# Kernel tuning notes

Hardware: AMD Instinct MI355X
Metric: run time of the kernel (lower is better)

Reference implementation:

```python
import jax, jax.numpy as jnp
import numpy as np

LRELU_SLOPE = 0.2
ACT_GAIN = np.float32(np.sqrt(2.0))  # bias_act lrelu gain in StyleGAN2


def _per_sample_conv3x3(x, w):
    """Grouped-conv-as-batch trick: per-sample 3x3 conv.
    x: [B, C, H, W], w: [B, O, C, 3, 3] -> [B, O, H, W] (padding=1)."""
    def one(xi, wi):
        return jax.lax.conv_general_dilated(
            xi[None], wi, window_strides=(1, 1), padding=[(1, 1), (1, 1)],
            dimension_numbers=('NCHW', 'OIHW', 'NCHW'))[0]
    return jax.vmap(one)(x, w)


def setup_inputs() -> dict:
    key = jax.random.key(0)
    ks = jax.random.split(key, 10)
    B, C, R, W_DIM, IMG_C = 16, 512, 64, 512, 3
    inv_sqrt_c = np.float32(1.0 / np.sqrt(W_DIM))
    return {
        'ws': jax.random.normal(ks[0], (B, 2, W_DIM), jnp.float32),
        'const': jax.random.normal(ks[1], (C, R, R), jnp.float32),
        'conv_w': jax.random.normal(ks[2], (C, C, 3, 3), jnp.float32),
        'conv_b': jnp.zeros((C,), jnp.float32),
        'conv_aff_w': jax.random.normal(ks[3], (C, W_DIM), jnp.float32) * inv_sqrt_c,
        'conv_aff_b': jnp.ones((C,), jnp.float32),
        'noise_const': jax.random.normal(ks[4], (R, R), jnp.float32),
        'noise_strength': jnp.full((1,), 0.1, jnp.float32),
        'rgb_w': jax.random.normal(ks[5], (IMG_C, C, 1, 1), jnp.float32),
        'rgb_b': jnp.zeros((IMG_C,), jnp.float32),
        'rgb_aff_w': jax.random.normal(ks[6], (C, W_DIM), jnp.float32) * inv_sqrt_c,
        'rgb_aff_b': jnp.ones((C,), jnp.float32),
    }


def reference(ws, const, conv_w, conv_b, conv_aff_w, conv_aff_b,
              noise_const, noise_strength, rgb_w, rgb_b, rgb_aff_w, rgb_aff_b):
    B = ws.shape[0]
    # const input broadcast to batch (in_channels == 0 block)
    x = jnp.broadcast_to(const[None], (B,) + const.shape)

    # --- SynthesisLayer: modulated_conv2d (demodulate=True, fused_modconv=True) ---
    s = ws[:, 0] @ conv_aff_w.T + conv_aff_b                    # [B, C] styles
    w = conv_w[None] * s[:, None, :, None, None]                # [B, O, C, 3, 3] modulate
    dcoefs = jax.lax.rsqrt(jnp.sum(jnp.square(w), axis=(2, 3, 4)) + 1e-8)  # [B, O]
    w = w * dcoefs[:, :, None, None, None]                      # demodulate
    x = _per_sample_conv3x3(x, w)                               # grouped conv trick
    x = x + noise_const[None, None] * noise_strength            # fused noise add
    x = jax.nn.leaky_relu(x + conv_b[None, :, None, None], LRELU_SLOPE) * ACT_GAIN

    # --- ToRGBLayer: modulated 1x1 conv, demodulate=False ---
    weight_gain = np.float32(1.0 / np.sqrt(conv_w.shape[1]))    # 1/sqrt(in_ch*kh*kw)
    s2 = (ws[:, 1] @ rgb_aff_w.T + rgb_aff_b) * weight_gain     # [B, C]
    img = jnp.einsum('bchw,oc,bc->bohw', x, rgb_w[:, :, 0, 0], s2)
    img = img + rgb_b[None, :, None, None]
    return x, img
```

## Files before the change

kernel.cpp:

```cpp
#include <hip/hip_runtime.h>
#include <hip/hip_bf16.h>

typedef __attribute__((ext_vector_type(8))) short short8;
typedef __attribute__((ext_vector_type(4))) float f32x4;

#define LRELU_SLOPE 0.2f
#define ACT_GAIN 1.41421356237309515f
#define WG_RGB 0.04419417382415922f

__device__ __forceinline__ void glds16(const short* g, short* l) {
    __builtin_amdgcn_global_load_lds(
        (const __attribute__((address_space(1))) unsigned int*)g,
        (__attribute__((address_space(3))) unsigned int*)l, 16, 0, 0);
}

__global__ void k_init(__hip_bfloat16* __restrict__ Ypad,
                       const float* __restrict__ rgb_b, float* __restrict__ img) {
    int blk = blockIdx.x, tid = threadIdx.x;
    if (blk < 1040) {
        int gslot = blk*4 + (tid >> 6);
        int b = gslot / 260;
        int cell = gslot - b*260;
        int h, w;
        if (cell < 66)       { h = 0;          w = cell; }
        else if (cell < 132) { h = 65;         w = cell - 66; }
        else if (cell < 196) { h = cell - 131; w = 0; }
        else                 { h = cell - 195; w = 65; }
        short8 z = {};
        *(short8*)((short*)Ypad + (((b*66 + h)*66) + w)*512 + (tid & 63)*8) = z;
    } else {
        int blk2 = blk - 1040;
        #pragma unroll
        for (int j = 0; j < 4; ++j) {
            int f4 = blk2*1024 + j*256 + tid;
            int b3 = f4 >> 10;
            int o3 = b3 % 3;
            float v = rgb_b[o3];
            f32x4 vv = {v, v, v, v};
            *(f32x4*)(img + f4*4) = vv;
        }
    }
}

__global__ void k_styles(const float* __restrict__ wsin,
                         const float* __restrict__ caw, const float* __restrict__ cab,
                         const float* __restrict__ raw_, const float* __restrict__ rab,
                         float* __restrict__ sbuf, float* __restrict__ s2buf) {
    int b = blockIdx.x, which = blockIdx.y;
    int tid = threadIdx.x, lane = tid & 63, wv = tid >> 6;
    const float* aw = which ? raw_ : caw;
    const float* ab = which ? rab : cab;
    float scale = which ? WG_RGB : 1.0f;
    float* op = which ? s2buf : sbuf;
    __shared__ float wsv[512];
    wsv[tid]       = wsin[(b*2 + which)*512 + tid];
    wsv[tid + 256] = wsin[(b*2 + which)*512 + tid + 256];
    __syncthreads();
    for (int c = wv; c < 512; c += 4) {
        float p = 0.f;
        #pragma unroll
        for (int kk = 0; kk < 8; ++kk)
            p += aw[c*512 + kk*64 + lane] * wsv[kk*64 + lane];
        #pragma unroll
        for (int off = 32; off; off >>= 1) p += __shfl_down(p, off, 64);
        if (lane == 0) op[b*512 + c] = (p + ab[c]) * scale;
    }
}

__global__ __launch_bounds__(256) void k_prepw(const float* __restrict__ conv_w,
                        float* __restrict__ w2sum, __hip_bfloat16* __restrict__ Abf) {
    int o = blockIdx.x, tid = threadIdx.x;
    __shared__ float wrow[4608];
    const f32x4* src = (const f32x4*)(conv_w + o*4608);
    #pragma unroll
    for (int r = 0; r < 5; ++r) {
        int idx = tid + (r << 8);
        if (idx < 1152) *(f32x4*)&wrow[idx*4] = src[idx];
    }
    __syncthreads();
    #pragma unroll
    for (int j = 0; j < 2; ++j) {
        int c = tid + (j << 8);
        float sum = 0.f;
        #pragma unroll
        for (int t = 0; t < 9; ++t) {
            float v = wrow[c*9 + t];
            sum += v*v;
            Abf[(t*512 + o)*512 + c] = __float2bfloat16(v);
        }
        w2sum[o*512 + c] = sum;
    }
}

__global__ __launch_bounds__(256) void k_dcoef(const float* __restrict__ sbuf,
                                               const float* __restrict__ w2sum,
                                               const float* __restrict__ s2buf,
                                               const float* __restrict__ rgb_w,
                                               float* __restrict__ dcoef,
                                               float* __restrict__ rgbc) {
    int gw = blockIdx.x*4 + (threadIdx.x >> 6);
    int lane = threadIdx.x & 63;
    int b = gw >> 9, o = gw & 511;
    float acc = 0.f;
    #pragma unroll
    for (int i = 0; i < 8; ++i) {
        int c = (i << 6) + lane;
        float sv = sbuf[(b << 9) + c];
        acc += sv*sv*w2sum[(o << 9) + c];
    }
    #pragma unroll
    for (int off = 32; off; off >>= 1) acc += __shfl_down(acc, off, 64);
    if (lane == 0) dcoef[(b << 9) + o] = rsqrtf(acc + 1e-8f);
    if (blockIdx.x < 96) {
        int flat = blockIdx.x*256 + threadIdx.x;
        int bb = flat / 1536;
        int r  = flat - bb*1536;
        int c  = r & 511;
        rgbc[flat] = rgb_w[r] * s2buf[bb*512 + c];
    }
}

__global__ void k_ypad(const float* __restrict__ cst, const float* __restrict__ sbuf,
                       __hip_bfloat16* __restrict__ Ypad) {
    int b = blockIdx.x >> 6, h = blockIdx.x & 63, tid = threadIdx.x;
    __shared__ float tile[64][65];
    for (int cc = 0; cc < 8; ++cc) {
        int c0 = cc << 6;
        #pragma unroll
        for (int it = 0; it < 16; ++it) {
            int cl = (it << 2) + (tid >> 6);
            int w = tid & 63;
            tile[cl][w] = cst[(c0 + cl)*4096 + (h << 6) + w];
        }
        __syncthreads();
        #pragma unroll
        for (int it = 0; it < 16; ++it) {
            int flat = (it << 8) + tid;
            int w = flat >> 6, cl = flat & 63;
            float v = sbuf[(b << 9) + c0 + cl] * tile[cl][w];
            Ypad[(((b*66 + h + 1)*66) + (w + 1))*512 + c0 + cl] = __float2bfloat16(v);
        }
        __syncthreads();
    }
}

__global__ __launch_bounds__(256, 2) void conv_gemm(
    const short* __restrict__ Abf,
    const short* __restrict__ Ypad,
    const float* __restrict__ dcoef,
    const float* __restrict__ noise,
    const float* __restrict__ nstr,
    const float* __restrict__ bias,
    const float* __restrict__ rgbc,
    float* __restrict__ xout,
    float* __restrict__ img)
{
    __shared__ short Aring[16384];
    __shared__ short Bh2[16896];
    __shared__ float red[128][3][2];
    int tid = threadIdx.x, lane = tid & 63, wv = tid >> 6;

    int blk = blockIdx.x;
    int xcd = blk & 7, idx = blk >> 3;
    int mblk = xcd & 3;
    int nblk = idx | ((xcd >> 2) << 8);
    int b  = nblk >> 5;
    int n0 = (nblk & 31) << 7;
    int o0 = mblk << 7;
    int h0 = n0 >> 6;

    int bgofs[4];
    #pragma unroll
    for (int r = 0; r < 4; ++r) {
        int i = tid + (r << 8);
        int p = i >> 2;
        int hl = p / 66;
        int w  = p - hl*66;
        int q  = (i & 3) ^ ((p >> 1) & 3);
        bgofs[r] = (((b*66 + h0 + hl)*66) + w)*512 + q*8;
    }
    int i4 = 1024 + (lane & 31);
    int p4 = i4 >> 2;
    int hl4 = p4 / 66;
    int w4 = p4 - hl4*66;
    int q4 = (i4 & 3) ^ ((p4 >> 1) & 3);
    int bgofs4 = (((b*66 + h0 + hl4)*66) + w4)*512 + q4*8;

    int aofs[2];
    #pragma unroll
    for (int r = 0; r < 2; ++r) {
        int s = tid + (r << 8);
        int row = s >> 2;
        int q = (s & 3) ^ ((row >> 1) & 3);
        aofs[r] = ((o0 + row) << 9) + q*8;
    }

    int quad = lane >> 4, ml = lane & 15;
    int sa = (quad ^ ((ml >> 1) & 3)) << 3;
    int mw = (wv & 1) << 6, nw = (wv >> 1) << 6;
    int nh = nw >> 6;
    short* BW0 = Bh2 + ((tid & ~63) << 3);
    short* AW0 = Aring + (wv << 9);

    f32x4 acc[4][4] = {};

    #pragma unroll
    for (int r = 0; r < 4; ++r) glds16(Ypad + bgofs[r], BW0 + (r << 11));
    if (lane < 32) glds16(Ypad + bgofs4, Bh2 + 8192);
    #pragma unroll
    for (int t = 0; t < 3; ++t) {
        glds16(Abf + (t << 18) + aofs[0], AW0 + t*4096);
        glds16(Abf + (t << 18) + aofs[1], AW0 + t*4096 + 2048);
    }
    asm volatile("s_waitcnt vmcnt(4)" ::: "memory");
    __builtin_amdgcn_s_barrier();

    for (int ch = 0; ch < 16; ++ch) {
        int c0 = ch << 5;
        int half = ch & 1;
        const short* Bbase = Bh2 + (half ? 8448 : 0);
        short* BWn  = Bh2 + (half ? 0 : 8448) + ((tid & ~63) << 3);
        short* Brem = Bh2 + (half ? 0 : 8448) + 8192;
        int c0n = (c0 + 32) & 511;
        int rb = ch & 3;
        #pragma unroll
        for (int tap = 0; tap < 9; ++tap) {
            int rr = (rb + tap) & 3;
            int rw = (rb + tap + 3) & 3;
            int tapP = (tap < 6) ? tap + 3 : tap - 6;
            int c0P  = (tap < 6) ? c0 : c0n;
            const short* asrc = Abf + (tapP << 18) + c0P;
            glds16(asrc + aofs[0], AW0 + rw*4096);
            glds16(asrc + aofs[1], AW0 + rw*4096 + 2048);
            if (tap < 4)
                glds16(Ypad + bgofs[tap] + c0n, BWn + (tap << 11));
            if (tap == 4) {
                if (lane < 32) glds16(Ypad + bgofs4 + c0n, Brem);
            }
            int dh = tap / 3, tl = tap % 3;
            const short* Ar = Aring + rr*4096;
            int pb = (nh + dh)*66 + ml + tl;
            int swz = (quad ^ ((pb >> 1) & 3)) << 3;
            short8 af[4], bf[4];
            #pragma unroll
            for (int i = 0; i < 4; ++i) {
                af[i] = *(const short8*)(Ar + (mw + ml + i*16)*32 + sa);
                bf[i] = *(const short8*)(Bbase + (pb + i*16)*32 + swz);
            }
            __builtin_amdgcn_s_setprio(1);
            #pragma unroll
            for (int mi = 0; mi < 4; ++mi)
                #pragma unroll
                for (int ni = 0; ni < 4; ++ni)
                    acc[mi][ni] = __builtin_amdgcn_mfma_f32_16x16x32_bf16(af[mi], bf[ni], acc[mi][ni], 0, 0, 0);
            __builtin_amdgcn_s_setprio(0);
            {
                constexpr int VM[9] = {5, 6, 7, 7, 7, 6, 5, 4, 4};
                asm volatile("s_waitcnt vmcnt(%0)" :: "i"(VM[tap]) : "memory");
            }
            __builtin_amdgcn_s_barrier();
        }
    }

    float ns = nstr[0];
    float pr[4][3] = {};
    #pragma unroll
    for (int mi = 0; mi < 4; ++mi) {
        int ob = o0 + mw + mi*16 + (quad << 2);
        f32x4 dc  = *(const f32x4*)(dcoef + (b << 9) + ob);
        f32x4 bs4 = *(const f32x4*)(bias + ob);
        f32x4 rc0 = *(const f32x4*)(rgbc + b*1536 + ob);
        f32x4 rc1 = *(const f32x4*)(rgbc + b*1536 + 512 + ob);
        f32x4 rc2 = *(const f32x4*)(rgbc + b*1536 + 1024 + ob);
        #pragma unroll
        for (int ni = 0; ni < 4; ++ni) {
            int hw = n0 + nw + ni*16 + ml;
            float nz = noise[hw] * ns;
            #pragma unroll
            for (int r = 0; r < 4; ++r) {
                float v = acc[mi][ni][r] * dc[r] + nz + bs4[r];
                v = (v < 0.0f ? LRELU_SLOPE * v : v) * ACT_GAIN;
                xout[(((b << 9) + ob + r) << 12) + hw] = v;
                pr[ni][0] += v * rc0[r];
                pr[ni][1] += v * rc1[r];
                pr[ni][2] += v * rc2[r];
            }
        }
    }
    #pragma unroll
    for (int ni = 0; ni < 4; ++ni)
        #pragma unroll
        for (int o3 = 0; o3 < 3; ++o3) {
            float v = pr[ni][o3];
            v += __shfl_down(v, 16, 64);
            v += __shfl_down(v, 32, 64);
            pr[ni][o3] = v;
        }
    if (lane < 16) {
        #pragma unroll
        for (int ni = 0; ni < 4; ++ni)
            #pragma unroll
            for (int o3 = 0; o3 < 3; ++o3)
                red[nw + ni*16 + ml][o3][wv & 1] = pr[ni][o3];
    }
    __syncthreads();
    for (int p = tid; p < 384; p += 256) {
        int o3 = p >> 7, hwl = p & 127;
        float v = red[hwl][o3][0] + red[hwl][o3][1];
        atomicAdd(img + ((b*3 + o3) << 12) + n0 + hwl, v);
    }
}

extern "C" void kernel_launch(void* const* d_in, const int* in_sizes, int n_in,
                              void* d_out, int out_size, void* d_ws, size_t ws_size,
                              hipStream_t stream) {
    (void)in_sizes; (void)n_in; (void)out_size; (void)ws_size;
    const float* wsin   = (const float*)d_in[0];
    const float* cst    = (const float*)d_in[1];
    const float* conv_w = (const float*)d_in[2];
    const float* conv_b = (const float*)d_in[3];
    const float* caw    = (const float*)d_in[4];
    const float* cab    = (const float*)d_in[5];
    const float* noise  = (const float*)d_in[6];
    const float* nstr   = (const float*)d_in[7];
    const float* rgb_w  = (const float*)d_in[8];
    const float* rgb_b  = (const float*)d_in[9];
    const float* raw_   = (const float*)d_in[10];
    const float* rab    = (const float*)d_in[11];

    char* wsb = (char*)d_ws;
    float* sbuf   = (float*)(wsb + 0);
    float* s2buf  = (float*)(wsb + 32768);
    float* dcoef  = (float*)(wsb + 65536);
    float* rgbc   = (float*)(wsb + 98304);
    float* w2sum  = (float*)(wsb + 196608);
    __hip_bfloat16* Abf  = (__hip_bfloat16*)(wsb + 1245184);
    __hip_bfloat16* Ypad = (__hip_bfloat16*)(wsb + 5963776);

    float* xout = (float*)d_out;
    float* img  = xout + 33554432;

    k_init<<<1088, 256, 0, stream>>>(Ypad, rgb_b, img);
    k_styles<<<dim3(16, 2), 256, 0, stream>>>(wsin, caw, cab, raw_, rab, sbuf, s2buf);
    k_prepw<<<512, 256, 0, stream>>>(conv_w, w2sum, Abf);
    k_dcoef<<<2048, 256, 0, stream>>>(sbuf, w2sum, s2buf, rgb_w, dcoef, rgbc);
    k_ypad<<<1024, 256, 0, stream>>>(cst, sbuf, Ypad);
    conv_gemm<<<2048, 256, 0, stream>>>((const short*)Abf, (const short*)Ypad,
                                        dcoef, noise, nstr, conv_b, rgbc, xout, img);
}
```

Before: 648.1 us.

## Double-buffer MFMA register fragments to overlap LDS reads with matrix math

Restructures the main conv GEMM loop so the LDS-to-register fragment loads for the next tap are issued before the MFMAs of the current tap, using two register fragment buffers. The channel loop is unrolled by two so buffer half pointers become compile-time constants, and a sched_barrier pins the ordering. The vmcnt wait thresholds are adjusted to match the new issue order. This targets LDS read latency that was exposed before each tap's MFMAs, at the cost of extra VGPRs and larger code.

Result: faster. 593.2 us (-8.5%).

```diff
diff --git a/kernel.cpp b/kernel.cpp
--- a/kernel.cpp
+++ b/kernel.cpp
@@ -186,81 +186,111 @@
     int q4 = (i4 & 3) ^ ((p4 >> 1) & 3);
     int bgofs4 = (((b*66 + h0 + hl4)*66) + w4)*512 + q4*8;
 
-    int aofs[2];
-    #pragma unroll
-    for (int r = 0; r < 2; ++r) {
-        int s = tid + (r << 8);
-        int row = s >> 2;
-        int q = (s & 3) ^ ((row >> 1) & 3);
-        aofs[r] = ((o0 + row) << 9) + q*8;
+    int aofs0, aofs1;
+    {
+        int s0 = tid,       r0 = s0 >> 2, q0 = (s0 & 3) ^ ((r0 >> 1) & 3);
+        int s1 = tid + 256, r1 = s1 >> 2, q1 = (s1 & 3) ^ ((r1 >> 1) & 3);
+        aofs0 = ((o0 + r0) << 9) + q0*8;
+        aofs1 = ((o0 + r1) << 9) + q1*8;
     }
 
     int quad = lane >> 4, ml = lane & 15;
     int sa = (quad ^ ((ml >> 1) & 3)) << 3;
     int mw = (wv & 1) << 6, nw = (wv >> 1) << 6;
     int nh = nw >> 6;
-    short* BW0 = Bh2 + ((tid & ~63) << 3);
+    const short* H0 = Bh2;
+    const short* H1 = Bh2 + 8448;
+    short* BW0h = Bh2 + ((tid & ~63) << 3);
+    short* BW1h = BW0h + 8448;
+    short* Brem0 = Bh2 + 8192;
+    short* Brem1 = Bh2 + 8448 + 8192;
     short* AW0 = Aring + (wv << 9);
 
     f32x4 acc[4][4] = {};
-
-    #pragma unroll
-    for (int r = 0; r < 4; ++r) glds16(Ypad + bgofs[r], BW0 + (r << 11));
-    if (lane < 32) glds16(Ypad + bgofs4, Bh2 + 8192);
+    short8 fa[2][4], fb[2][4];
+
+    #pragma unroll
+    for (int r = 0; r < 4; ++r) glds16(Ypad + bgofs[r], BW0h + (r << 11));
+    if (lane < 32) glds16(Ypad + bgofs4, Brem0);
     #pragma unroll
     for (int t = 0; t < 3; ++t) {
-        glds16(Abf + (t << 18) + aofs[0], AW0 + t*4096);
-        glds16(Abf + (t << 18) + aofs[1], AW0 + t*4096 + 2048);
-    }
-    asm volatile("s_waitcnt vmcnt(4)" ::: "memory");
+        glds16(Abf + (t << 18) + aofs0, AW0 + t*4096);
+        glds16(Abf + (t << 18) + aofs1, AW0 + t*4096 + 2048);
+    }
+    asm volatile("s_waitcnt vmcnt(2)" ::: "memory");
     __builtin_amdgcn_s_barrier();
-
-    for (int ch = 0; ch < 16; ++ch) {
-        int c0 = ch << 5;
-        int half = ch & 1;
-        const short* Bbase = Bh2 + (half ? 8448 : 0);
-        short* BWn  = Bh2 + (half ? 0 : 8448) + ((tid & ~63) << 3);
-        short* Brem = Bh2 + (half ? 0 : 8448) + 8192;
-        int c0n = (c0 + 32) & 511;
-        int rb = ch & 3;
-        #pragma unroll
-        for (int tap = 0; tap < 9; ++tap) {
-            int rr = (rb + tap) & 3;
-            int rw = (rb + tap + 3) & 3;
-            int tapP = (tap < 6) ? tap + 3 : tap - 6;
-            int c0P  = (tap < 6) ? c0 : c0n;
-            const short* asrc = Abf + (tapP << 18) + c0P;
-            glds16(asrc + aofs[0], AW0 + rw*4096);
-            glds16(asrc + aofs[1], AW0 + rw*4096 + 2048);
-            if (tap < 4)
-                glds16(Ypad + bgofs[tap] + c0n, BWn + (tap << 11));
-            if (tap == 4) {
-                if (lane < 32) glds16(Ypad + bgofs4 + c0n, Brem);
-            }
-            int dh = tap / 3, tl = tap % 3;
-            const short* Ar = Aring + rr*4096;
-            int pb = (nh + dh)*66 + ml + tl;
-            int swz = (quad ^ ((pb >> 1) & 3)) << 3;
-            short8 af[4], bf[4];
-            #pragma unroll
-            for (int i = 0; i < 4; ++i) {
-                af[i] = *(const short8*)(Ar + (mw + ml + i*16)*32 + sa);
-                bf[i] = *(const short8*)(Bbase + (pb + i*16)*32 + swz);
-            }
-            __builtin_amdgcn_s_setprio(1);
-            #pragma unroll
-            for (int mi = 0; mi < 4; ++mi)
-                #pragma unroll
-                for (int ni = 0; ni < 4; ++ni)
-                    acc[mi][ni] = __builtin_amdgcn_mfma_f32_16x16x32_bf16(af[mi], bf[ni], acc[mi][ni], 0, 0, 0);
-            __builtin_amdgcn_s_setprio(0);
-            {
-                constexpr int VM[9] = {5, 6, 7, 7, 7, 6, 5, 4, 4};
-                asm volatile("s_waitcnt vmcnt(%0)" :: "i"(VM[tap]) : "memory");
-            }
-            __builtin_amdgcn_s_barrier();
-        }
-    }
+    {
+        int pb0 = nh*66 + ml;
+        int swz0 = (quad ^ ((pb0 >> 1) & 3)) << 3;
+        #pragma unroll
+        for (int i = 0; i < 4; ++i) {
+            fa[0][i] = *(const short8*)(Aring + (mw + ml + i*16)*32 + sa);
+            fb[0][i] = *(const short8*)(H0 + (pb0 + i*16)*32 + swz0);
+        }
+    }
+
+    constexpr int VMP[9] = {3, 4, 4, 4, 4, 3, 2, 2, 2};
+
+#define PHASE(TAP, CUR, C0, C0N, RB, BC, BN, BWN, BRM)                          \
+    {                                                                           \
+        constexpr int TAPN = ((TAP) + 1) % 9;                                   \
+        constexpr int NXT = (CUR) ^ 1;                                          \
+                                           \
+        int rrN = ((RB) + (TAP) + 1) & 3;                                       \
+        const short* ArN = Aring + rrN*4096;                                    \
+        const short* BbN = ((TAP) == 8) ? (BN) : (BC);                          \
+        int pbN = (nh + TAPN/3)*66 + ml + TAPN%3;                               \
+        int swzN = (quad ^ ((pbN >> 1) & 3)) << 3;                              \
+        _Pragma("unroll")                                                       \
+        for (int i = 0; i < 4; ++i) {                                           \
+            fa[NXT][i] = *(const short8*)(ArN + (mw + ml + i*16)*32 + sa);      \
+            fb[NXT][i] = *(const short8*)(BbN + (pbN + i*16)*32 + swzN);        \
+        }                                                                       \
+                \
+        {                                                                       \
+            constexpr int TAPP = ((TAP) < 6) ? (TAP) + 3 : (TAP) - 6;           \
+            const short* asrc = Abf + (TAPP << 18) + (((TAP) < 6) ? (C0) : (C0N)); \
+            int rw = ((RB) + (TAP) + 3) & 3;                                    \
+            glds16(asrc + aofs0, AW0 + rw*4096);                                \
+            glds16(asrc + aofs1, AW0 + rw*4096 + 2048);                         \
+        }                                                                       \
+        if ((TAP) < 4) glds16(Ypad + bgofs[(TAP)] + (C0N), (BWN) + ((TAP) << 11)); \
+        if ((TAP) == 4) { if (lane < 32) glds16(Ypad + bgofs4 + (C0N), (BRM)); } \
+        __builtin_amdgcn_sched_barrier(0);                                      \
+        __builtin_amdgcn_s_setprio(1);                                          \
+        _Pragma("unroll")                                                       \
+        for (int mi = 0; mi < 4; ++mi)                                          \
+            _Pragma("unroll")                                                   \
+            for (int ni = 0; ni < 4; ++ni)                                      \
+                acc[mi][ni] = __builtin_amdgcn_mfma_f32_16x16x32_bf16(          \
+                    fa[(CUR)][mi], fb[(CUR)][ni], acc[mi][ni], 0, 0, 0);        \
+        __builtin_amdgcn_s_setprio(0);                                          \
+        asm volatile("s_waitcnt vmcnt(%0)" :: "i"(VMP[(TAP)]) : "memory");      \
+        __builtin_amdgcn_s_barrier();                                           \
+    }
+
+#define CHUNK9(PAR, C0, C0N, RB, BC, BN, BWN, BRM)                              \
+    PHASE(0, ((0 + (PAR)) & 1), C0, C0N, RB, BC, BN, BWN, BRM)                  \
+    PHASE(1, ((1 + (PAR)) & 1), C0, C0N, RB, BC, BN, BWN, BRM)                  \
+    PHASE(2, ((2 + (PAR)) & 1), C0, C0N, RB, BC, BN, BWN, BRM)                  \
+    PHASE(3, ((3 + (PAR)) & 1), C0, C0N, RB, BC, BN, BWN, BRM)                  \
+    PHASE(4, ((4 + (PAR)) & 1), C0, C0N, RB, BC, BN, BWN, BRM)                  \
+    PHASE(5, ((5 + (PAR)) & 1), C0, C0N, RB, BC, BN, BWN, BRM)                  \
+    PHASE(6, ((6 + (PAR)) & 1), C0, C0N, RB, BC, BN, BWN, BRM)                  \
+    PHASE(7, ((7 + (PAR)) & 1), C0, C0N, RB, BC, BN, BWN, BRM)                  \
+    PHASE(8, ((8 + (PAR)) & 1), C0, C0N, RB, BC, BN, BWN, BRM)
+
+    for (int cc = 0; cc < 8; ++cc) {
+        int c0e = cc << 6;
+        int rbe = (cc << 1) & 3;
+        CHUNK9(0, c0e, c0e + 32, rbe, H0, H1, BW1h, Brem1)
+        int c0o = c0e + 32;
+        int c0no = (c0e + 64) & 511;
+        int rbo = (rbe + 1) & 3;
+        CHUNK9(1, c0o, c0no, rbo, H1, H0, BW0h, Brem0)
+    }
+#undef PHASE
+#undef CHUNK9
 
     float ns = nstr[0];
     float pr[4][3] = {};
```

## Enlarge conv GEMM tiles to 256x256 with 32x32 MFMA and fragment double-buffering

Applied to the files above, without the earlier changes.

Restructures the implicit-GEMM conv kernel from 128x128 tiles with 4 waves to 256x256 tiles with 8 waves (512 threads, 512 blocks). It switches from 16x16x32 to 32x32x16 bf16 MFMA and splits each tap into two K-halves whose LDS fragment loads are double-buffered against the MFMAs. The goal is higher arithmetic intensity per LDS and global byte and better latency hiding. In exchange it needs much more LDS and register pressure (acc now 128 floats per lane), and the grid has fewer blocks per CU.

Result: faster. 574.3 us (-11.4%).

```diff
diff --git a/kernel.cpp b/kernel.cpp
--- a/kernel.cpp
+++ b/kernel.cpp
@@ -3,6 +3,7 @@
 
 typedef __attribute__((ext_vector_type(8))) short short8;
 typedef __attribute__((ext_vector_type(4))) float f32x4;
+typedef __attribute__((ext_vector_type(16))) float f32x16;
 
 #define LRELU_SLOPE 0.2f
 #define ACT_GAIN 1.41421356237309515f
@@ -144,7 +145,7 @@
     }
 }
 
-__global__ __launch_bounds__(256, 2) void conv_gemm(
+__global__ __launch_bounds__(512, 2) void conv_gemm(
     const short* __restrict__ Abf,
     const short* __restrict__ Ypad,
     const float* __restrict__ dcoef,
@@ -155,159 +156,216 @@
     float* __restrict__ xout,
     float* __restrict__ img)
 {
-    __shared__ short Aring[16384];
-    __shared__ short Bh2[16896];
-    __shared__ float red[128][3][2];
+    __shared__ short Aring[32768];
+    __shared__ short Bh2[25344];
+    __shared__ float red[256][3][2];
+
     int tid = threadIdx.x, lane = tid & 63, wv = tid >> 6;
+    int wr = wv >> 2, wc = wv & 3;
+    int ml32 = lane & 31, hi = lane >> 5;
 
     int blk = blockIdx.x;
     int xcd = blk & 7, idx = blk >> 3;
-    int mblk = xcd & 3;
-    int nblk = idx | ((xcd >> 2) << 8);
-    int b  = nblk >> 5;
-    int n0 = (nblk & 31) << 7;
-    int o0 = mblk << 7;
-    int h0 = n0 >> 6;
-
-    int bgofs[4];
-    #pragma unroll
-    for (int r = 0; r < 4; ++r) {
-        int i = tid + (r << 8);
-        int p = i >> 2;
-        int hl = p / 66;
-        int w  = p - hl*66;
-        int q  = (i & 3) ^ ((p >> 1) & 3);
-        bgofs[r] = (((b*66 + h0 + hl)*66) + w)*512 + q*8;
-    }
-    int i4 = 1024 + (lane & 31);
-    int p4 = i4 >> 2;
-    int hl4 = p4 / 66;
-    int w4 = p4 - hl4*66;
-    int q4 = (i4 & 3) ^ ((p4 >> 1) & 3);
-    int bgofs4 = (((b*66 + h0 + hl4)*66) + w4)*512 + q4*8;
-
-    int aofs[2];
+    int v = xcd * 64 + idx;
+    int mblk = v & 1, nblk = v >> 1;
+    int b = nblk >> 4;
+    int hw0 = (nblk & 15) << 8;
+    int h0 = hw0 >> 6;
+    int o0 = mblk << 8;
+
+    int bgofs[3];
+    #pragma unroll
+    for (int r = 0; r < 3; ++r) {
+        int i = tid + (r << 9);
+        int pos = i >> 2;
+        int hl = pos / 66;
+        int ww = pos - hl*66;
+        int q  = (i & 3) ^ ((pos >> 1) & 3);
+        bgofs[r] = (((b*66 + h0 + hl)*66) + ww)*512 + q*8;
+    }
+    int pos4 = 384 + (lane >> 2);
+    int q4 = (lane & 3) ^ ((pos4 >> 1) & 3);
+    int bg4 = ((b*66 + h0 + 5)*66 + (pos4 - 330))*512 + q4*8;
+
+    int agofs[2];
     #pragma unroll
     for (int r = 0; r < 2; ++r) {
-        int s = tid + (r << 8);
+        int s = tid + (r << 9);
         int row = s >> 2;
         int q = (s & 3) ^ ((row >> 1) & 3);
-        aofs[r] = ((o0 + row) << 9) + q*8;
-    }
-
-    int quad = lane >> 4, ml = lane & 15;
-    int sa = (quad ^ ((ml >> 1) & 3)) << 3;
-    int mw = (wv & 1) << 6, nw = (wv >> 1) << 6;
-    int nh = nw >> 6;
-    short* BW0 = Bh2 + ((tid & ~63) << 3);
-    short* AW0 = Aring + (wv << 9);
-
-    f32x4 acc[4][4] = {};
-
-    #pragma unroll
-    for (int r = 0; r < 4; ++r) glds16(Ypad + bgofs[r], BW0 + (r << 11));
-    if (lane < 32) glds16(Ypad + bgofs4, Bh2 + 8192);
+        agofs[r] = ((o0 + row) << 9) + q*8;
+    }
+
+    int aro[4], arx[4];
+    #pragma unroll
+    for (int mi = 0; mi < 4; ++mi) {
+        int row = wr*128 + mi*32 + ml32;
+        aro[mi] = row*32;
+        arx[mi] = (row >> 1) & 3;
+    }
+    int pb0 = wc*66 + ml32;
+    const int BPA[9] = {0, 1, 2, 66, 67, 68, 132, 133, 134};
+
+    short* AW = Aring + wv*512;
+
+    f32x16 acc[4][2] = {};
+    short8 fa0[4], fb0[2], fa1[4], fb1[2];
+
+    #pragma unroll
+    for (int r = 0; r < 3; ++r)
+        glds16(Ypad + bgofs[r], Bh2 + wv*512 + r*4096);
+    if (lane < 48) glds16(Ypad + bg4, Bh2 + 12288);
     #pragma unroll
     for (int t = 0; t < 3; ++t) {
-        glds16(Abf + (t << 18) + aofs[0], AW0 + t*4096);
-        glds16(Abf + (t << 18) + aofs[1], AW0 + t*4096 + 2048);
-    }
-    asm volatile("s_waitcnt vmcnt(4)" ::: "memory");
+        glds16(Abf + (t << 18) + agofs[0], AW + t*8192);
+        glds16(Abf + (t << 18) + agofs[1], AW + t*8192 + 4096);
+    }
+    asm volatile("s_waitcnt vmcnt(2)" ::: "memory");
     __builtin_amdgcn_s_barrier();
-
-    for (int ch = 0; ch < 16; ++ch) {
-        int c0 = ch << 5;
-        int half = ch & 1;
-        const short* Bbase = Bh2 + (half ? 8448 : 0);
-        short* BWn  = Bh2 + (half ? 0 : 8448) + ((tid & ~63) << 3);
-        short* Brem = Bh2 + (half ? 0 : 8448) + 8192;
-        int c0n = (c0 + 32) & 511;
-        int rb = ch & 3;
-        #pragma unroll
-        for (int tap = 0; tap < 9; ++tap) {
-            int rr = (rb + tap) & 3;
-            int rw = (rb + tap + 3) & 3;
-            int tapP = (tap < 6) ? tap + 3 : tap - 6;
-            int c0P  = (tap < 6) ? c0 : c0n;
-            const short* asrc = Abf + (tapP << 18) + c0P;
-            glds16(asrc + aofs[0], AW0 + rw*4096);
-            glds16(asrc + aofs[1], AW0 + rw*4096 + 2048);
-            if (tap < 4)
-                glds16(Ypad + bgofs[tap] + c0n, BWn + (tap << 11));
-            if (tap == 4) {
-                if (lane < 32) glds16(Ypad + bgofs4 + c0n, Brem);
-            }
-            int dh = tap / 3, tl = tap % 3;
-            const short* Ar = Aring + rr*4096;
-            int pb = (nh + dh)*66 + ml + tl;
-            int swz = (quad ^ ((pb >> 1) & 3)) << 3;
-            short8 af[4], bf[4];
-            #pragma unroll
-            for (int i = 0; i < 4; ++i) {
-                af[i] = *(const short8*)(Ar + (mw + ml + i*16)*32 + sa);
-                bf[i] = *(const short8*)(Bbase + (pb + i*16)*32 + swz);
-            }
-            __builtin_amdgcn_s_setprio(1);
-            #pragma unroll
-            for (int mi = 0; mi < 4; ++mi)
-                #pragma unroll
-                for (int ni = 0; ni < 4; ++ni)
-                    acc[mi][ni] = __builtin_amdgcn_mfma_f32_16x16x32_bf16(af[mi], bf[ni], acc[mi][ni], 0, 0, 0);
-            __builtin_amdgcn_s_setprio(0);
-            {
-                constexpr int VM[9] = {5, 6, 7, 7, 7, 6, 5, 4, 4};
-                asm volatile("s_waitcnt vmcnt(%0)" :: "i"(VM[tap]) : "memory");
-            }
-            __builtin_amdgcn_s_barrier();
-        }
-    }
+    {
+        int pos_ = pb0;
+        int x_ = (pos_ >> 1) & 3;
+        #pragma unroll
+        for (int mi = 0; mi < 4; ++mi)
+            fa0[mi] = *(const short8*)(Aring + aro[mi] + ((hi ^ arx[mi]) << 3));
+        #pragma unroll
+        for (int ni = 0; ni < 2; ++ni)
+            fb0[ni] = *(const short8*)(Bh2 + (pos_ + ni*32)*32 + ((hi ^ x_) << 3));
+    }
+
+    const int VMP[9] = {3, 4, 4, 4, 3, 2, 2, 2, 2};
+
+#define MMCL(FA, FB)                                                            \
+    __builtin_amdgcn_s_setprio(1);                                              \
+    _Pragma("unroll")                                                           \
+    for (int mi = 0; mi < 4; ++mi)                                              \
+        _Pragma("unroll")                                                       \
+        for (int ni = 0; ni < 2; ++ni)                                          \
+            acc[mi][ni] = __builtin_amdgcn_mfma_f32_32x32x16_bf16(              \
+                FA[mi], FB[ni], acc[mi][ni], 0, 0, 0);                          \
+    __builtin_amdgcn_s_setprio(0);
+
+#define PHASE(TAP, HC, C0, C0N, RB)                                             \
+    {                                                                           \
+        int rr  = ((RB) + (TAP)) & 3;                                           \
+        int rrN = ((RB) + (TAP) + 1) & 3;                                       \
+        int rw  = ((RB) + (TAP) + 3) & 3;                                       \
+        constexpr int TAPN = ((TAP) + 1) % 9;                                   \
+        constexpr int TAPP = ((TAP) < 6) ? (TAP) + 3 : (TAP) - 6;               \
+        constexpr int HN = (HC) ^ 1;                                            \
+        constexpr int HRA = ((TAP) == 8) ? HN : (HC);                           \
+                                  \
+        { int pos_ = pb0 + BPA[(TAP)]; int x_ = (pos_ >> 1) & 3;                \
+          _Pragma("unroll")                                                     \
+          for (int mi = 0; mi < 4; ++mi)                                        \
+              fa1[mi] = *(const short8*)(Aring + rr*8192 + aro[mi]              \
+                                         + (((2 + hi) ^ arx[mi]) << 3));        \
+          _Pragma("unroll")                                                     \
+          for (int ni = 0; ni < 2; ++ni)                                        \
+              fb1[ni] = *(const short8*)(Bh2 + (HC)*12672 + (pos_ + ni*32)*32   \
+                                         + (((2 + hi) ^ x_) << 3));             \
+        }                                                                       \
+                         \
+        { const short* asrc_ = Abf + (TAPP << 18) + (((TAP) < 6) ? (C0) : (C0N)); \
+          glds16(asrc_ + agofs[0], AW + rw*8192);                               \
+          glds16(asrc_ + agofs[1], AW + rw*8192 + 4096); }                      \
+        if ((TAP) < 3)                                                          \
+            glds16(Ypad + bgofs[(TAP)] + (C0N),                                 \
+                   Bh2 + HN*12672 + wv*512 + (TAP)*4096);                       \
+        if ((TAP) == 3) {                                                       \
+            if (lane < 48) glds16(Ypad + bg4 + (C0N), Bh2 + HN*12672 + 12288);  \
+        }                                                                       \
+        __builtin_amdgcn_sched_barrier(0);                                      \
+        MMCL(fa0, fb0)                                                          \
+        __builtin_amdgcn_sched_barrier(0);                                      \
+                                \
+        { int pos_ = pb0 + BPA[TAPN]; int x_ = (pos_ >> 1) & 3;                 \
+          _Pragma("unroll")                                                     \
+          for (int mi = 0; mi < 4; ++mi)                                        \
+              fa0[mi] = *(const short8*)(Aring + rrN*8192 + aro[mi]             \
+                                         + ((hi ^ arx[mi]) << 3));              \
+          _Pragma("unroll")                                                     \
+          for (int ni = 0; ni < 2; ++ni)                                        \
+              fb0[ni] = *(const short8*)(Bh2 + HRA*12672 + (pos_ + ni*32)*32    \
+                                         + ((hi ^ x_) << 3));                   \
+        }                                                                       \
+        __builtin_amdgcn_sched_barrier(0);                                      \
+        MMCL(fa1, fb1)                                                          \
+        asm volatile("s_waitcnt vmcnt(%0)" :: "i"(VMP[(TAP)]) : "memory");      \
+        __builtin_amdgcn_s_barrier();                                           \
+    }
+
+#define CHUNK9(HC, C0, C0N, RB)                                                 \
+    PHASE(0, HC, C0, C0N, RB) PHASE(1, HC, C0, C0N, RB)                         \
+    PHASE(2, HC, C0, C0N, RB) PHASE(3, HC, C0, C0N, RB)                         \
+    PHASE(4, HC, C0, C0N, RB) PHASE(5, HC, C0, C0N, RB)                         \
+    PHASE(6, HC, C0, C0N, RB) PHASE(7, HC, C0, C0N, RB)                         \
+    PHASE(8, HC, C0, C0N, RB)
+
+    for (int cc = 0; cc < 8; ++cc) {
+        int c0e = cc << 6;
+        int rbe = (cc << 1) & 3;
+        CHUNK9(0, c0e, c0e + 32, rbe)
+        int c0o = c0e + 32;
+        int c0no = (c0e + 64) & 511;
+        int rbo = (rbe + 1) & 3;
+        CHUNK9(1, c0o, c0no, rbo)
+    }
+#undef PHASE
+#undef CHUNK9
+#undef MMCL
 
     float ns = nstr[0];
-    float pr[4][3] = {};
+    float pr0[2] = {0.f, 0.f}, pr1[2] = {0.f, 0.f}, pr2[2] = {0.f, 0.f};
     #pragma unroll
     for (int mi = 0; mi < 4; ++mi) {
-        int ob = o0 + mw + mi*16 + (quad << 2);
-        f32x4 dc  = *(const f32x4*)(dcoef + (b << 9) + ob);
-        f32x4 bs4 = *(const f32x4*)(bias + ob);
-        f32x4 rc0 = *(const f32x4*)(rgbc + b*1536 + ob);
-        f32x4 rc1 = *(const f32x4*)(rgbc + b*1536 + 512 + ob);
-        f32x4 rc2 = *(const f32x4*)(rgbc + b*1536 + 1024 + ob);
-        #pragma unroll
-        for (int ni = 0; ni < 4; ++ni) {
-            int hw = n0 + nw + ni*16 + ml;
+        int ob = o0 + wr*128 + mi*32 + hi*4;
+        f32x4 dc[4], bs[4], c0r[4], c1r[4], c2r[4];
+        #pragma unroll
+        for (int g = 0; g < 4; ++g) {
+            dc[g]  = *(const f32x4*)(dcoef + (b << 9) + ob + g*8);
+            bs[g]  = *(const f32x4*)(bias + ob + g*8);
+            c0r[g] = *(const f32x4*)(rgbc + b*1536 + ob + g*8);
+            c1r[g] = *(const f32x4*)(rgbc + b*1536 + 512 + ob + g*8);
+            c2r[g] = *(const f32x4*)(rgbc + b*1536 + 1024 + ob + g*8);
+        }
+        #pragma unroll
+        for (int ni = 0; ni < 2; ++ni) {
+            int nl = wc*64 + ni*32 + ml32;
+            int hw = hw0 + nl;
             float nz = noise[hw] * ns;
             #pragma unroll
-            for (int r = 0; r < 4; ++r) {
-                float v = acc[mi][ni][r] * dc[r] + nz + bs4[r];
-                v = (v < 0.0f ? LRELU_SLOPE * v : v) * ACT_GAIN;
-                xout[(((b << 9) + ob + r) << 12) + hw] = v;
-                pr[ni][0] += v * rc0[r];
-                pr[ni][1] += v * rc1[r];
-                pr[ni][2] += v * rc2[r];
-            }
-        }
-    }
-    #pragma unroll
-    for (int ni = 0; ni < 4; ++ni)
-        #pragma unroll
-        for (int o3 = 0; o3 < 3; ++o3) {
-            float v = pr[ni][o3];
-            v += __shfl_down(v, 16, 64);
-            v += __shfl_down(v, 32, 64);
-            pr[ni][o3] = v;
-        }
-    if (lane < 16) {
-        #pragma unroll
-        for (int ni = 0; ni < 4; ++ni)
-            #pragma unroll
-            for (int o3 = 0; o3 < 3; ++o3)
-                red[nw + ni*16 + ml][o3][wv & 1] = pr[ni][o3];
+            for (int g = 0; g < 4; ++g)
+                #pragma unroll
+                for (int t = 0; t < 4; ++t) {
+                    float vv = acc[mi][ni][g*4 + t] * dc[g][t] + nz + bs[g][t];
+                    vv = (vv < 0.f ? LRELU_SLOPE*vv : vv) * ACT_GAIN;
+                    xout[(((b << 9) + ob + g*8 + t) << 12) + hw] = vv;
+                    pr0[ni] += vv * c0r[g][t];
+                    pr1[ni] += vv * c1r[g][t];
+                    pr2[ni] += vv * c2r[g][t];
+                }
+        }
+    }
+    #pragma unroll
+    for (int ni = 0; ni < 2; ++ni) {
+        pr0[ni] += __shfl_down(pr0[ni], 32, 64);
+        pr1[ni] += __shfl_down(pr1[ni], 32, 64);
+        pr2[ni] += __shfl_down(pr2[ni], 32, 64);
+    }
+    if (lane < 32) {
+        #pragma unroll
+        for (int ni = 0; ni < 2; ++ni) {
+            int nl = wc*64 + ni*32 + ml32;
+            red[nl][0][wr] = pr0[ni];
+            red[nl][1][wr] = pr1[ni];
+            red[nl][2][wr] = pr2[ni];
+        }
     }
     __syncthreads();
-    for (int p = tid; p < 384; p += 256) {
-        int o3 = p >> 7, hwl = p & 127;
-        float v = red[hwl][o3][0] + red[hwl][o3][1];
-        atomicAdd(img + ((b*3 + o3) << 12) + n0 + hwl, v);
+    for (int p = tid; p < 768; p += 512) {
+        int o3 = p >> 8, nl = p & 255;
+        atomicAdd(img + ((b*3 + o3) << 12) + hw0 + nl, red[nl][o3][0] + red[nl][o3][1]);
     }
 }
 
@@ -345,6 +403,6 @@
     k_prepw<<<512, 256, 0, stream>>>(conv_w, w2sum, Abf);
     k_dcoef<<<2048, 256, 0, stream>>>(sbuf, w2sum, s2buf, rgb_w, dcoef, rgbc);
     k_ypad<<<1024, 256, 0, stream>>>(cst, sbuf, Ypad);
-    conv_gemm<<<2048, 256, 0, stream>>>((const short*)Abf, (const short*)Ypad,
-                                        dcoef, noise, nstr, conv_b, rgbc, xout, img);
-}
+    conv_gemm<<<512, 512, 0, stream>>>((const short*)Abf, (const short*)Ypad,
+                                       dcoef, noise, nstr, conv_b, rgbc, xout, img);
+}
```
